# Performance work log

Measured on AMD Instinct MI355X. Metric: run time of the kernel, lower is better.

The kernel has to match this reference:

```python
import jax, jax.numpy as jnp
import numpy as np

D_MODEL = 512
N_HEAD = 8
D_K = 64
EPS = 1e-5


def setup_inputs() -> dict:
    key = jax.random.key(0)
    ks = jax.random.split(key, 12)
    B, S = 4, 2048
    Q = jax.random.normal(ks[0], (B, S, D_MODEL), dtype=jnp.float32)
    K = jax.random.normal(ks[1], (B, S, D_MODEL), dtype=jnp.float32)
    V = jax.random.normal(ks[2], (B, S, D_MODEL), dtype=jnp.float32)
    # bool padding-style mask: True = masked position
    att_mask = jax.random.randint(ks[3], (B, S, S), 0, 2).astype(bool)
    s = 1.0 / np.sqrt(D_MODEL)
    # Linear weights stored as [in, out] (transpose of torch's [out, in]; same math)
    Wq = jax.random.uniform(ks[4], (D_MODEL, N_HEAD * D_K), jnp.float32, -s, s)
    bq = jax.random.uniform(ks[5], (N_HEAD * D_K,), jnp.float32, -s, s)
    Wk = jax.random.uniform(ks[6], (D_MODEL, N_HEAD * D_K), jnp.float32, -s, s)
    bk = jax.random.uniform(ks[7], (N_HEAD * D_K,), jnp.float32, -s, s)
    Wv = jax.random.uniform(ks[8], (D_MODEL, N_HEAD * D_K), jnp.float32, -s, s)
    bv = jax.random.uniform(ks[9], (N_HEAD * D_K,), jnp.float32, -s, s)
    Wo = jax.random.uniform(ks[10], (N_HEAD * D_K, D_MODEL), jnp.float32, -s, s)
    bo = jax.random.uniform(ks[11], (D_MODEL,), jnp.float32, -s, s)
    return {"Q": Q, "K": K, "V": V, "att_mask": att_mask,
            "Wq": Wq, "bq": bq, "Wk": Wk, "bk": bk,
            "Wv": Wv, "bv": bv, "Wo": Wo, "bo": bo}


def _layer_norm(x):
    # nn.LayerNorm with default weight=1, bias=0 (fresh module in forward)
    mu = jnp.mean(x, axis=-1, keepdims=True)
    var = jnp.mean(jnp.square(x - mu), axis=-1, keepdims=True)
    return (x - mu) / jnp.sqrt(var + EPS)


def reference(Q, K, V, att_mask, Wq, bq, Wk, bk, Wv, bv, Wo, bo):
    B, S, _ = Q.shape
    residual = Q
    # QKV projections -> [B, H, S, Dk]
    q = (Q @ Wq + bq).reshape(B, S, N_HEAD, D_K).transpose(0, 2, 1, 3)
    k = (K @ Wk + bk).reshape(B, S, N_HEAD, D_K).transpose(0, 2, 1, 3)
    v = (V @ Wv + bv).reshape(B, S, N_HEAD, D_K).transpose(0, 2, 1, 3)
    # scaled dot-product attention with padding mask
    score = jnp.einsum('bhqd,bhkd->bhqk', q, k) / np.sqrt(D_K)
    score = jnp.where(att_mask[:, None, :, :], jnp.float32(-1e9), score)
    attn = jax.nn.softmax(score, axis=-1)
    context = jnp.einsum('bhqk,bhkd->bhqd', attn, v)
    context = context.transpose(0, 2, 1, 3).reshape(B, S, N_HEAD * D_K)
    output = context @ Wo + bo
    out = _layer_norm(output + residual)
    return out, attn
```

## Files before the change

kernel.cpp:

```cpp
#include <hip/hip_runtime.h>
#include <hip/hip_bf16.h>
#include <cstdint>
#include <cstddef>


typedef __attribute__((ext_vector_type(8)))  short short8v;
typedef __attribute__((ext_vector_type(2)))  float f32x2;
typedef __attribute__((ext_vector_type(4)))  float f32x4;
typedef __attribute__((ext_vector_type(16))) float f32x16;

constexpr int DM = 512, S = 2048, BATCH = 4, NHEAD = 8, DK = 64;
constexpr int ROWS = BATCH * S;
constexpr int BH   = BATCH * NHEAD;
constexpr size_t OUT_ELEMS = (size_t)ROWS * DM;
constexpr size_t HFRAG = 131072;

#define ZERO16 {0.f,0.f,0.f,0.f,0.f,0.f,0.f,0.f,0.f,0.f,0.f,0.f,0.f,0.f,0.f,0.f}

__device__ __forceinline__ unsigned short f2bf(float f) {
    union { __hip_bfloat16 b; unsigned short u; } c;
    c.b = __float2bfloat16(f);
    return c.u;
}
__device__ __forceinline__ float bf2f(unsigned short u) {
    union { float f; unsigned u32; } c;
    c.u32 = (unsigned)u << 16;
    return c.f;
}

__global__ __launch_bounds__(256)
void wconv(const float* __restrict__ Wq, const float* __restrict__ Wk,
           const float* __restrict__ Wv, const float* __restrict__ Wo,
           unsigned short* __restrict__ wt)
{
    __shared__ float T[32][33];
    const float* srcs[4] = {Wq, Wk, Wv, Wo};
    const float* W = srcs[blockIdx.z];
    unsigned short* out = wt + (size_t)blockIdx.z * DM * DM;
    const int r0 = blockIdx.y * 32, c0 = blockIdx.x * 32;
    const int tid = threadIdx.x;
#pragma unroll
    for (int i = 0; i < 4; ++i) {
        int lin = tid + i * 256; int r = lin >> 5, c = lin & 31;
        T[r][c] = W[(size_t)(r0 + r) * DM + c0 + c];
    }
    __syncthreads();
#pragma unroll
    for (int i = 0; i < 4; ++i) {
        int lin = tid + i * 256; int rn = lin >> 5, ck = lin & 31;
        out[(size_t)(c0 + rn) * DM + r0 + ck] = f2bf(T[ck][rn]);
    }
}

__global__ __launch_bounds__(256)
void maskpack(const uint8_t* __restrict__ mask, unsigned* __restrict__ mb)
{
    const int t = threadIdx.x;
    const int row = blockIdx.x * 4 + (t >> 6);
    const int w = t & 63;
    const uint8_t* src = mask + (size_t)row * S + 32 * w;
    const uint4 a = *reinterpret_cast<const uint4*>(src);
    const uint4 b = *reinterpret_cast<const uint4*>(src + 16);
    const unsigned m8[8] = {a.x, a.y, a.z, a.w, b.x, b.y, b.z, b.w};
    unsigned bits = 0;
#pragma unroll
    for (int k2 = 0; k2 < 32; ++k2)
        bits |= (((m8[k2 >> 2] >> (8 * (k2 & 3))) & 0xffu) ? 1u : 0u) << k2;
    mb[(size_t)row * 64 + w] = bits;
}

__global__ __launch_bounds__(256)
void proj3_mfma(const float* __restrict__ Qin, const float* __restrict__ Kin,
                const float* __restrict__ Vin, const unsigned short* __restrict__ wt,
                const float* __restrict__ bq, const float* __restrict__ bk,
                const float* __restrict__ bv,
                unsigned short* __restrict__ qo, unsigned short* __restrict__ ko,
                unsigned short* __restrict__ vo)
{
    const int z = blockIdx.z;
    const float* X = (z == 0) ? Qin : (z == 1) ? Kin : Vin;
    const unsigned short* Wt = wt + (size_t)z * DM * DM;
    const float* bias = (z == 0) ? bq : (z == 1) ? bk : bv;
    unsigned short* Y = (z == 0) ? qo : (z == 1) ? ko : vo;
    const float scale = (z == 0) ? 0.125f : 1.0f;

    const int tid = threadIdx.x, wv = tid >> 6, l = tid & 63, lr = l & 31, lh = l >> 5;
    const int m0 = blockIdx.y * 128 + wv * 32;
    const int n0 = blockIdx.x * 64;
    const float* xp = X + (size_t)(m0 + lr) * DM + 8 * lh;
    const unsigned short* w0 = Wt + (size_t)(n0 + lr) * DM + 8 * lh;
    const unsigned short* w1 = w0 + (size_t)32 * DM;
    f32x16 acc0 = ZERO16, acc1 = ZERO16;
#pragma unroll 8
    for (int t = 0; t < 32; ++t) {
        float4 xa = *reinterpret_cast<const float4*>(xp + 16 * t);
        float4 xb = *reinterpret_cast<const float4*>(xp + 16 * t + 4);
        short8v a;
        a[0] = (short)f2bf(xa.x * scale); a[1] = (short)f2bf(xa.y * scale);
        a[2] = (short)f2bf(xa.z * scale); a[3] = (short)f2bf(xa.w * scale);
        a[4] = (short)f2bf(xb.x * scale); a[5] = (short)f2bf(xb.y * scale);
        a[6] = (short)f2bf(xb.z * scale); a[7] = (short)f2bf(xb.w * scale);
        short8v b0 = *reinterpret_cast<const short8v*>(w0 + 16 * t);
        short8v b1 = *reinterpret_cast<const short8v*>(w1 + 16 * t);
        acc0 = __builtin_amdgcn_mfma_f32_32x32x16_bf16(a, b0, acc0, 0, 0, 0);
        acc1 = __builtin_amdgcn_mfma_f32_32x32x16_bf16(a, b1, acc1, 0, 0, 0);
    }
#pragma unroll
    for (int j = 0; j < 2; ++j) {
        const f32x16 acc = j ? acc1 : acc0;
        const int n = n0 + 32 * j + lr;
        const float bvv = bias[n] * scale;
        const int h = n >> 6, d = n & 63;
#pragma unroll
        for (int r = 0; r < 16; ++r) {
            const int m = m0 + (r & 3) + 8 * (r >> 2) + 4 * lh;
            const int bb = m >> 11, s = m & (S - 1);
            const int bh = bb * NHEAD + h;
            const unsigned short val = f2bf(acc[r] + bvv);
            size_t idx;
            if (z == 0)
                idx = ((size_t)bh * S + s) * DK + d;
            else if (z == 1)
                idx = (size_t)bh * HFRAG + (size_t)(s >> 4) * 1024 + (size_t)(d >> 5) * 512
                      + (size_t)(((s & 15) + 16 * ((d & 31) >> 3)) << 3) + (d & 7);
            else
                idx = (size_t)bh * HFRAG + (size_t)(s >> 5) * 2048 + (size_t)(d >> 4) * 512
                      + (size_t)(((d & 15) + 16 * ((s & 31) >> 3)) << 3) + (s & 7);
            Y[idx] = val;
        }
    }
}

__global__ __launch_bounds__(512)
void attn_fused(const unsigned short* __restrict__ q,
                const unsigned short* __restrict__ kpack,
                const unsigned short* __restrict__ vpack,
                const unsigned* __restrict__ mbits,
                float* __restrict__ attn,
                unsigned short* __restrict__ ctx)
{
    __shared__ char Pc[16 * 4096];
    __shared__ float cred[2][4][16][16];
    const int tid = threadIdx.x, wv = tid >> 6, l = tid & 63;
    const int lq = l & 15, lg = l >> 4;
    const int bh = blockIdx.y, q0 = blockIdx.x * 16;
    const int b = bh >> 3, h = bh & 7;

    const unsigned short* qp = q + ((size_t)bh * S + q0 + lq) * DK + 8 * lg;
    const short8v af0 = *reinterpret_cast<const short8v*>(qp);
    const short8v af1 = *reinterpret_cast<const short8v*>(qp + 32);
    const unsigned short* kbase = kpack + (size_t)bh * HFRAG + (size_t)l * 8;
#pragma unroll 4
    for (int it = 0; it < 16; ++it) {
        const int c = it * 8 + wv;
        const unsigned short* kc = kbase + (size_t)c * 1024;
        const short8v b0 = *reinterpret_cast<const short8v*>(kc);
        const short8v b1 = *reinterpret_cast<const short8v*>(kc + 512);
        f32x4 acc = {0.f, 0.f, 0.f, 0.f};
        acc = __builtin_amdgcn_mfma_f32_16x16x32_bf16(af0, b0, acc, 0, 0, 0);
        acc = __builtin_amdgcn_mfma_f32_16x16x32_bf16(af1, b1, acc, 0, 0, 0);
        const int col = c * 16 + lq;
#pragma unroll
        for (int r = 0; r < 4; ++r) {
            const int row = lg * 4 + r;
            *reinterpret_cast<unsigned short*>(
                Pc + row * 4096 + ((2 * col) ^ ((row & 7) << 4))) = f2bf(acc[r]);
        }
    }
    __syncthreads();

#pragma unroll
    for (int rr = 0; rr < 2; ++rr) {
        const int row = wv * 2 + rr;
        const int grow = q0 + row;
        const int swz = (row & 7) << 4;
        const unsigned mk = mbits[((size_t)b * S + grow) * 64 + l];
        float xs[4][8];
        float vmax = -1e30f;
#pragma unroll
        for (int i = 0; i < 4; ++i) {
            const int c = 4 * l + i;
            const short8v pr = *reinterpret_cast<const short8v*>(
                Pc + row * 4096 + ((16 * c) ^ swz));
#pragma unroll
            for (int j = 0; j < 8; ++j) {
                const bool masked = (mk >> (8 * i + j)) & 1u;
                xs[i][j] = masked ? -1e30f : bf2f((unsigned short)pr[j]);
                vmax = fmaxf(vmax, xs[i][j]);
            }
        }
#pragma unroll
        for (int off = 32; off; off >>= 1) vmax = fmaxf(vmax, __shfl_xor(vmax, off));
        float sum = 0.f;
#pragma unroll
        for (int i = 0; i < 4; ++i)
#pragma unroll
            for (int j = 0; j < 8; ++j) {
                xs[i][j] = __expf(xs[i][j] - vmax);
                sum += xs[i][j];
            }
#pragma unroll
        for (int off = 32; off; off >>= 1) sum += __shfl_xor(sum, off);
        const float inv = 1.0f / sum;
#pragma unroll
        for (int i = 0; i < 4; ++i) {
            const int c = 4 * l + i;
            ushort4 p0, p1;
            p0.x = f2bf(xs[i][0] * inv); p0.y = f2bf(xs[i][1] * inv);
            p0.z = f2bf(xs[i][2] * inv); p0.w = f2bf(xs[i][3] * inv);
            p1.x = f2bf(xs[i][4] * inv); p1.y = f2bf(xs[i][5] * inv);
            p1.z = f2bf(xs[i][6] * inv); p1.w = f2bf(xs[i][7] * inv);
            char* pb = Pc + row * 4096 + ((16 * c) ^ swz);
            *reinterpret_cast<ushort4*>(pb)     = p0;
            *reinterpret_cast<ushort4*>(pb + 8) = p1;
        }
    }
    __syncthreads();

    const int dt = wv & 3, kh = wv >> 2;
    const int rswz = (lq & 7) << 4;
    f32x4 acc = {0.f, 0.f, 0.f, 0.f};
    const unsigned short* vbase = vpack + (size_t)bh * HFRAG + dt * 512 + (size_t)l * 8;
    const int wrow = 8 * kh + 2 * dt + (l >> 5);
    const int wswz = (wrow & 7) << 4;
    const int lc = l & 31;
    float* arow = attn + ((size_t)bh * S + q0 + wrow) * S;
#pragma unroll 4
    for (int s = 0; s < 32; ++s) {
        const int kk0 = kh * 1024 + 32 * s;
        const short8v a = *reinterpret_cast<const short8v*>(
            Pc + lq * 4096 + ((2 * (kk0 + 8 * lg)) ^ rswz));
        const short8v bf = *reinterpret_cast<const short8v*>(
            vbase + (size_t)(kh * 32 + s) * 2048);
        acc = __builtin_amdgcn_mfma_f32_16x16x32_bf16(a, bf, acc, 0, 0, 0);
        const unsigned pw = *reinterpret_cast<const unsigned*>(
            Pc + wrow * 4096 + ((128 * s + 4 * lc) ^ wswz));
        f32x2 st;
        st[0] = bf2f((unsigned short)(pw & 0xffffu));
        st[1] = bf2f((unsigned short)(pw >> 16));
        __builtin_nontemporal_store(st,
            reinterpret_cast<f32x2*>(arow + 64 * s + 2 * lc));
    }
#pragma unroll
    for (int r = 0; r < 4; ++r) cred[kh][dt][lg * 4 + r][lq] = acc[r];
    __syncthreads();

    for (int o = tid; o < 1024; o += 512) {
        const int qq = o >> 6, dd = o & 63;
        const float val = cred[0][dd >> 4][qq][dd & 15] + cred[1][dd >> 4][qq][dd & 15];
        ctx[((size_t)(b * S + q0 + qq)) * DM + h * DK + dd] = f2bf(val);
    }
}

__global__ __launch_bounds__(256)
void out_mfma(const unsigned short* __restrict__ Xc, const unsigned short* __restrict__ Wt,
              const float* __restrict__ bias, const float* __restrict__ resid,
              float* __restrict__ pre)
{
    const int tid = threadIdx.x, wv = tid >> 6, l = tid & 63, lr = l & 31, lh = l >> 5;
    const int m0 = blockIdx.y * 128 + wv * 32;
    const int n0 = blockIdx.x * 64;
    const unsigned short* xp = Xc + (size_t)(m0 + lr) * DM + 8 * lh;
    const unsigned short* w0 = Wt + (size_t)(n0 + lr) * DM + 8 * lh;
    const unsigned short* w1 = w0 + (size_t)32 * DM;
    f32x16 acc0 = ZERO16, acc1 = ZERO16;
#pragma unroll 8
    for (int t = 0; t < 32; ++t) {
        short8v a  = *reinterpret_cast<const short8v*>(xp + 16 * t);
        short8v b0 = *reinterpret_cast<const short8v*>(w0 + 16 * t);
        short8v b1 = *reinterpret_cast<const short8v*>(w1 + 16 * t);
        acc0 = __builtin_amdgcn_mfma_f32_32x32x16_bf16(a, b0, acc0, 0, 0, 0);
        acc1 = __builtin_amdgcn_mfma_f32_32x32x16_bf16(a, b1, acc1, 0, 0, 0);
    }
#pragma unroll
    for (int j = 0; j < 2; ++j) {
        const f32x16 acc = j ? acc1 : acc0;
        const int n = n0 + 32 * j + lr;
        const float bv = bias[n];
#pragma unroll
        for (int r = 0; r < 16; ++r) {
            const int m = m0 + (r & 3) + 8 * (r >> 2) + 4 * lh;
            pre[(size_t)m * DM + n] = acc[r] + bv + resid[(size_t)m * DM + n];
        }
    }
}

__global__ __launch_bounds__(128)
void ln_kernel(const float* __restrict__ pre, float* __restrict__ out)
{
    const size_t row = blockIdx.x;
    const int tid = threadIdx.x;
    const int wave = tid >> 6;
    float4 x = reinterpret_cast<const float4*>(pre + row * DM)[tid];

    float s = x.x + x.y + x.z + x.w;
#pragma unroll
    for (int off = 32; off; off >>= 1) s += __shfl_xor(s, off);
    __shared__ float r1[2];
    if ((tid & 63) == 0) r1[wave] = s;
    __syncthreads();
    const float mean = (r1[0] + r1[1]) * (1.0f / 512.0f);

    float dx = x.x - mean, dy = x.y - mean, dz = x.z - mean, dw = x.w - mean;
    float sq = dx * dx + dy * dy + dz * dz + dw * dw;
#pragma unroll
    for (int off = 32; off; off >>= 1) sq += __shfl_xor(sq, off);
    __shared__ float r2[2];
    if ((tid & 63) == 0) r2[wave] = sq;
    __syncthreads();
    const float var = (r2[0] + r2[1]) * (1.0f / 512.0f);
    const float inv = rsqrtf(var + 1e-5f);

    float4 y;
    y.x = dx * inv; y.y = dy * inv; y.z = dz * inv; y.w = dw * inv;
    reinterpret_cast<float4*>(out + row * DM)[tid] = y;
}

extern "C" void kernel_launch(void* const* d_in, const int* in_sizes, int n_in,
                              void* d_out, int out_size, void* d_ws, size_t ws_size,
                              hipStream_t stream)
{
    (void)in_sizes; (void)n_in; (void)out_size; (void)ws_size;

    const float*   Qin  = (const float*)d_in[0];
    const float*   Kin  = (const float*)d_in[1];
    const float*   Vin  = (const float*)d_in[2];
    const uint8_t* mask = (const uint8_t*)d_in[3];
    const float*   Wq   = (const float*)d_in[4];
    const float*   bq   = (const float*)d_in[5];
    const float*   Wk   = (const float*)d_in[6];
    const float*   bk   = (const float*)d_in[7];
    const float*   Wv   = (const float*)d_in[8];
    const float*   bv   = (const float*)d_in[9];
    const float*   Wo   = (const float*)d_in[10];
    const float*   bo   = (const float*)d_in[11];

    float* out  = (float*)d_out;
    float* attn = out + OUT_ELEMS;

    char* w = (char*)d_ws;
    const size_t MB = 1 << 20;
    unsigned short* wt    = (unsigned short*)(w);
    unsigned short* qbf   = (unsigned short*)(w + 2  * MB);
    unsigned short* kpack = (unsigned short*)(w + 10 * MB);
    unsigned short* vpack = (unsigned short*)(w + 18 * MB);
    unsigned short* ctx   = (unsigned short*)(w + 26 * MB);
    float*          pre   = (float*)(w + 34 * MB);
    unsigned*       mbits = (unsigned*)(w + 50 * MB);

    unsigned short* wto = wt + 3 * (size_t)DM * DM;

    wconv<<<dim3(16, 16, 4), 256, 0, stream>>>(Wq, Wk, Wv, Wo, wt);

    maskpack<<<ROWS / 4, 256, 0, stream>>>(mask, mbits);

    proj3_mfma<<<dim3(DM / 64, ROWS / 128, 3), 256, 0, stream>>>(
        Qin, Kin, Vin, wt, bq, bk, bv, qbf, kpack, vpack);

    attn_fused<<<dim3(S / 16, BH), 512, 0, stream>>>(qbf, kpack, vpack, mbits, attn, ctx);

    out_mfma<<<dim3(DM / 64, ROWS / 128), 256, 0, stream>>>(ctx, wto, bo, Qin, pre);

    ln_kernel<<<ROWS, 128, 0, stream>>>(pre, out);
}
```

Baseline: 325.5 us.

## Keep attention scores in registers and fuse output projection with LayerNorm

The attention kernel now computes QK^T with K as the A operand, so each wave holds a 16x256 slice of scores in registers. Masking and softmax run in registers, with a cross-wave max/sum reduction through small shared arrays. The fp32 attention probabilities are written directly from registers, which drops the bf16 round-trip through LDS and the extra pass that reloaded scores for the store. Separately, the output projection and LayerNorm are fused into one kernel that covers a full 512-wide row per block, removing the fp32 pre-activation buffer. Variance now comes from a single pass as E[x^2]-mean^2, which carries some cancellation risk, and the 64 accumulator registers per lane may add register pressure despite the launch-bounds hint.

```diff
diff --git a/kernel.cpp b/kernel.cpp
--- a/kernel.cpp
+++ b/kernel.cpp
@@ -131,7 +131,7 @@
     }
 }
 
-__global__ __launch_bounds__(512)
+__global__ __launch_bounds__(512, 4)
 void attn_fused(const unsigned short* __restrict__ q,
                 const unsigned short* __restrict__ kpack,
                 const unsigned short* __restrict__ vpack,
@@ -141,90 +141,90 @@
 {
     __shared__ char Pc[16 * 4096];
     __shared__ float cred[2][4][16][16];
+    __shared__ float redm[8][16];
+    __shared__ float reds[8][16];
     const int tid = threadIdx.x, wv = tid >> 6, l = tid & 63;
     const int lq = l & 15, lg = l >> 4;
     const int bh = blockIdx.y, q0 = blockIdx.x * 16;
     const int b = bh >> 3, h = bh & 7;
 
     const unsigned short* qp = q + ((size_t)bh * S + q0 + lq) * DK + 8 * lg;
-    const short8v af0 = *reinterpret_cast<const short8v*>(qp);
-    const short8v af1 = *reinterpret_cast<const short8v*>(qp + 32);
+    const short8v qf0 = *reinterpret_cast<const short8v*>(qp);
+    const short8v qf1 = *reinterpret_cast<const short8v*>(qp + 32);
     const unsigned short* kbase = kpack + (size_t)bh * HFRAG + (size_t)l * 8;
-#pragma unroll 4
+    f32x4 acc[16];
+#pragma unroll
     for (int it = 0; it < 16; ++it) {
-        const int c = it * 8 + wv;
-        const unsigned short* kc = kbase + (size_t)c * 1024;
-        const short8v b0 = *reinterpret_cast<const short8v*>(kc);
-        const short8v b1 = *reinterpret_cast<const short8v*>(kc + 512);
-        f32x4 acc = {0.f, 0.f, 0.f, 0.f};
-        acc = __builtin_amdgcn_mfma_f32_16x16x32_bf16(af0, b0, acc, 0, 0, 0);
-        acc = __builtin_amdgcn_mfma_f32_16x16x32_bf16(af1, b1, acc, 0, 0, 0);
-        const int col = c * 16 + lq;
+        const unsigned short* kc = kbase + (size_t)(16 * wv + it) * 1024;
+        const short8v kf0 = *reinterpret_cast<const short8v*>(kc);
+        const short8v kf1 = *reinterpret_cast<const short8v*>(kc + 512);
+        f32x4 a = {0.f, 0.f, 0.f, 0.f};
+        a = __builtin_amdgcn_mfma_f32_16x16x32_bf16(kf0, qf0, a, 0, 0, 0);
+        a = __builtin_amdgcn_mfma_f32_16x16x32_bf16(kf1, qf1, a, 0, 0, 0);
+        acc[it] = a;
+    }
+
+    const unsigned* mrow = mbits + ((size_t)b * S + q0 + lq) * 64 + 8 * wv;
+    const uint4 mwa = *reinterpret_cast<const uint4*>(mrow);
+    const uint4 mwb = *reinterpret_cast<const uint4*>(mrow + 4);
+    const unsigned mw[8] = {mwa.x, mwa.y, mwa.z, mwa.w, mwb.x, mwb.y, mwb.z, mwb.w};
+    float vmax = -3e38f;
+#pragma unroll
+    for (int it = 0; it < 16; ++it) {
+        const unsigned word = mw[it >> 1] >> (16 * (it & 1) + 4 * lg);
 #pragma unroll
         for (int r = 0; r < 4; ++r) {
-            const int row = lg * 4 + r;
-            *reinterpret_cast<unsigned short*>(
-                Pc + row * 4096 + ((2 * col) ^ ((row & 7) << 4))) = f2bf(acc[r]);
+            const float v = ((word >> r) & 1u) ? -1e30f : acc[it][r];
+            acc[it][r] = v;
+            vmax = fmaxf(vmax, v);
         }
     }
-    __syncthreads();
-
-#pragma unroll
-    for (int rr = 0; rr < 2; ++rr) {
-        const int row = wv * 2 + rr;
-        const int grow = q0 + row;
-        const int swz = (row & 7) << 4;
-        const unsigned mk = mbits[((size_t)b * S + grow) * 64 + l];
-        float xs[4][8];
-        float vmax = -1e30f;
-#pragma unroll
-        for (int i = 0; i < 4; ++i) {
-            const int c = 4 * l + i;
-            const short8v pr = *reinterpret_cast<const short8v*>(
-                Pc + row * 4096 + ((16 * c) ^ swz));
-#pragma unroll
-            for (int j = 0; j < 8; ++j) {
-                const bool masked = (mk >> (8 * i + j)) & 1u;
-                xs[i][j] = masked ? -1e30f : bf2f((unsigned short)pr[j]);
-                vmax = fmaxf(vmax, xs[i][j]);
-            }
+    vmax = fmaxf(vmax, __shfl_xor(vmax, 16));
+    vmax = fmaxf(vmax, __shfl_xor(vmax, 32));
+    if (l < 16) redm[wv][l] = vmax;
+    __syncthreads();
+    float rmax = redm[0][lq];
+#pragma unroll
+    for (int w2 = 1; w2 < 8; ++w2) rmax = fmaxf(rmax, redm[w2][lq]);
+
+    float sum = 0.f;
+#pragma unroll
+    for (int it = 0; it < 16; ++it)
+#pragma unroll
+        for (int r = 0; r < 4; ++r) {
+            const float v = __expf(acc[it][r] - rmax);
+            acc[it][r] = v;
+            sum += v;
         }
-#pragma unroll
-        for (int off = 32; off; off >>= 1) vmax = fmaxf(vmax, __shfl_xor(vmax, off));
-        float sum = 0.f;
-#pragma unroll
-        for (int i = 0; i < 4; ++i)
-#pragma unroll
-            for (int j = 0; j < 8; ++j) {
-                xs[i][j] = __expf(xs[i][j] - vmax);
-                sum += xs[i][j];
-            }
-#pragma unroll
-        for (int off = 32; off; off >>= 1) sum += __shfl_xor(sum, off);
-        const float inv = 1.0f / sum;
-#pragma unroll
-        for (int i = 0; i < 4; ++i) {
-            const int c = 4 * l + i;
-            ushort4 p0, p1;
-            p0.x = f2bf(xs[i][0] * inv); p0.y = f2bf(xs[i][1] * inv);
-            p0.z = f2bf(xs[i][2] * inv); p0.w = f2bf(xs[i][3] * inv);
-            p1.x = f2bf(xs[i][4] * inv); p1.y = f2bf(xs[i][5] * inv);
-            p1.z = f2bf(xs[i][6] * inv); p1.w = f2bf(xs[i][7] * inv);
-            char* pb = Pc + row * 4096 + ((16 * c) ^ swz);
-            *reinterpret_cast<ushort4*>(pb)     = p0;
-            *reinterpret_cast<ushort4*>(pb + 8) = p1;
-        }
+    sum += __shfl_xor(sum, 16);
+    sum += __shfl_xor(sum, 32);
+    if (l < 16) reds[wv][l] = sum;
+    __syncthreads();
+    float rsum = 0.f;
+#pragma unroll
+    for (int w2 = 0; w2 < 8; ++w2) rsum += reds[w2][lq];
+    const float inv = 1.0f / rsum;
+
+    float* arow = attn + ((size_t)bh * S + q0 + lq) * S + 256 * wv;
+    const int swz = (lq & 7) << 4;
+    char* prow = Pc + lq * 4096;
+#pragma unroll
+    for (int it = 0; it < 16; ++it) {
+        const int n = 16 * it + 4 * lg;
+        f32x4 o;
+        o[0] = acc[it][0] * inv; o[1] = acc[it][1] * inv;
+        o[2] = acc[it][2] * inv; o[3] = acc[it][3] * inv;
+        __builtin_nontemporal_store(o, reinterpret_cast<f32x4*>(arow + n));
+        ushort4 p;
+        p.x = f2bf(o[0]); p.y = f2bf(o[1]); p.z = f2bf(o[2]); p.w = f2bf(o[3]);
+        *reinterpret_cast<ushort4*>(prow + ((2 * (256 * wv + n)) ^ swz)) = p;
     }
     __syncthreads();
 
     const int dt = wv & 3, kh = wv >> 2;
     const int rswz = (lq & 7) << 4;
-    f32x4 acc = {0.f, 0.f, 0.f, 0.f};
+    f32x4 pacc = {0.f, 0.f, 0.f, 0.f};
     const unsigned short* vbase = vpack + (size_t)bh * HFRAG + dt * 512 + (size_t)l * 8;
-    const int wrow = 8 * kh + 2 * dt + (l >> 5);
-    const int wswz = (wrow & 7) << 4;
-    const int lc = l & 31;
-    float* arow = attn + ((size_t)bh * S + q0 + wrow) * S;
 #pragma unroll 4
     for (int s = 0; s < 32; ++s) {
         const int kk0 = kh * 1024 + 32 * s;
@@ -232,17 +232,10 @@
             Pc + lq * 4096 + ((2 * (kk0 + 8 * lg)) ^ rswz));
         const short8v bf = *reinterpret_cast<const short8v*>(
             vbase + (size_t)(kh * 32 + s) * 2048);
-        acc = __builtin_amdgcn_mfma_f32_16x16x32_bf16(a, bf, acc, 0, 0, 0);
-        const unsigned pw = *reinterpret_cast<const unsigned*>(
-            Pc + wrow * 4096 + ((128 * s + 4 * lc) ^ wswz));
-        f32x2 st;
-        st[0] = bf2f((unsigned short)(pw & 0xffffu));
-        st[1] = bf2f((unsigned short)(pw >> 16));
-        __builtin_nontemporal_store(st,
-            reinterpret_cast<f32x2*>(arow + 64 * s + 2 * lc));
-    }
-#pragma unroll
-    for (int r = 0; r < 4; ++r) cred[kh][dt][lg * 4 + r][lq] = acc[r];
+        pacc = __builtin_amdgcn_mfma_f32_16x16x32_bf16(a, bf, pacc, 0, 0, 0);
+    }
+#pragma unroll
+    for (int r = 0; r < 4; ++r) cred[kh][dt][lg * 4 + r][lq] = pacc[r];
     __syncthreads();
 
     for (int o = tid; o < 1024; o += 512) {
@@ -252,14 +245,16 @@
     }
 }
 
-__global__ __launch_bounds__(256)
-void out_mfma(const unsigned short* __restrict__ Xc, const unsigned short* __restrict__ Wt,
-              const float* __restrict__ bias, const float* __restrict__ resid,
-              float* __restrict__ pre)
-{
+__global__ __launch_bounds__(512)
+void out_ln(const unsigned short* __restrict__ Xc, const unsigned short* __restrict__ Wt,
+            const float* __restrict__ bias, const float* __restrict__ resid,
+            float* __restrict__ out)
+{
+    __shared__ f32x2 red[32][8];
+    __shared__ f32x2 stat[32];
     const int tid = threadIdx.x, wv = tid >> 6, l = tid & 63, lr = l & 31, lh = l >> 5;
-    const int m0 = blockIdx.y * 128 + wv * 32;
-    const int n0 = blockIdx.x * 64;
+    const int m0 = blockIdx.x * 32;
+    const int n0 = wv * 64;
     const unsigned short* xp = Xc + (size_t)(m0 + lr) * DM + 8 * lh;
     const unsigned short* w0 = Wt + (size_t)(n0 + lr) * DM + 8 * lh;
     const unsigned short* w1 = w0 + (size_t)32 * DM;
@@ -272,48 +267,41 @@
         acc0 = __builtin_amdgcn_mfma_f32_32x32x16_bf16(a, b0, acc0, 0, 0, 0);
         acc1 = __builtin_amdgcn_mfma_f32_32x32x16_bf16(a, b1, acc1, 0, 0, 0);
     }
-#pragma unroll
-    for (int j = 0; j < 2; ++j) {
-        const f32x16 acc = j ? acc1 : acc0;
-        const int n = n0 + 32 * j + lr;
-        const float bv = bias[n];
-#pragma unroll
-        for (int r = 0; r < 16; ++r) {
-            const int m = m0 + (r & 3) + 8 * (r >> 2) + 4 * lh;
-            pre[(size_t)m * DM + n] = acc[r] + bv + resid[(size_t)m * DM + n];
+    const float bv0 = bias[n0 + lr], bv1 = bias[n0 + 32 + lr];
+#pragma unroll
+    for (int r = 0; r < 16; ++r) {
+        const int mloc = (r & 3) + 8 * (r >> 2) + 4 * lh;
+        const size_t mbase = (size_t)(m0 + mloc) * DM + n0 + lr;
+        const float v0 = acc0[r] + bv0 + resid[mbase];
+        const float v1 = acc1[r] + bv1 + resid[mbase + 32];
+        acc0[r] = v0; acc1[r] = v1;
+        float s = v0 + v1, sq = v0 * v0 + v1 * v1;
+#pragma unroll
+        for (int off = 16; off; off >>= 1) {
+            s  += __shfl_xor(s, off);
+            sq += __shfl_xor(sq, off);
         }
-    }
-}
-
-__global__ __launch_bounds__(128)
-void ln_kernel(const float* __restrict__ pre, float* __restrict__ out)
-{
-    const size_t row = blockIdx.x;
-    const int tid = threadIdx.x;
-    const int wave = tid >> 6;
-    float4 x = reinterpret_cast<const float4*>(pre + row * DM)[tid];
-
-    float s = x.x + x.y + x.z + x.w;
-#pragma unroll
-    for (int off = 32; off; off >>= 1) s += __shfl_xor(s, off);
-    __shared__ float r1[2];
-    if ((tid & 63) == 0) r1[wave] = s;
-    __syncthreads();
-    const float mean = (r1[0] + r1[1]) * (1.0f / 512.0f);
-
-    float dx = x.x - mean, dy = x.y - mean, dz = x.z - mean, dw = x.w - mean;
-    float sq = dx * dx + dy * dy + dz * dz + dw * dw;
-#pragma unroll
-    for (int off = 32; off; off >>= 1) sq += __shfl_xor(sq, off);
-    __shared__ float r2[2];
-    if ((tid & 63) == 0) r2[wave] = sq;
-    __syncthreads();
-    const float var = (r2[0] + r2[1]) * (1.0f / 512.0f);
-    const float inv = rsqrtf(var + 1e-5f);
-
-    float4 y;
-    y.x = dx * inv; y.y = dy * inv; y.z = dz * inv; y.w = dw * inv;
-    reinterpret_cast<float4*>(out + row * DM)[tid] = y;
+        if (lr == 0) { f32x2 t2; t2[0] = s; t2[1] = sq; red[mloc][wv] = t2; }
+    }
+    __syncthreads();
+    if (tid < 32) {
+        float s = 0.f, sq = 0.f;
+#pragma unroll
+        for (int w2 = 0; w2 < 8; ++w2) { s += red[tid][w2][0]; sq += red[tid][w2][1]; }
+        const float mean = s * (1.0f / 512.0f);
+        const float var = sq * (1.0f / 512.0f) - mean * mean;
+        f32x2 t2; t2[0] = mean; t2[1] = rsqrtf(var + 1e-5f);
+        stat[tid] = t2;
+    }
+    __syncthreads();
+#pragma unroll
+    for (int r = 0; r < 16; ++r) {
+        const int mloc = (r & 3) + 8 * (r >> 2) + 4 * lh;
+        const f32x2 st = stat[mloc];
+        const size_t mbase = (size_t)(m0 + mloc) * DM + n0 + lr;
+        out[mbase]      = (acc0[r] - st[0]) * st[1];
+        out[mbase + 32] = (acc1[r] - st[0]) * st[1];
+    }
 }
 
 extern "C" void kernel_launch(void* const* d_in, const int* in_sizes, int n_in,
@@ -345,8 +333,7 @@
     unsigned short* kpack = (unsigned short*)(w + 10 * MB);
     unsigned short* vpack = (unsigned short*)(w + 18 * MB);
     unsigned short* ctx   = (unsigned short*)(w + 26 * MB);
-    float*          pre   = (float*)(w + 34 * MB);
-    unsigned*       mbits = (unsigned*)(w + 50 * MB);
+    unsigned*       mbits = (unsigned*)(w + 34 * MB);
 
     unsigned short* wto = wt + 3 * (size_t)DM * DM;
 
@@ -359,7 +346,5 @@
 
     attn_fused<<<dim3(S / 16, BH), 512, 0, stream>>>(qbf, kpack, vpack, mbits, attn, ctx);
 
-    out_mfma<<<dim3(DM / 64, ROWS / 128), 256, 0, stream>>>(ctx, wto, bo, Qin, pre);
-
-    ln_kernel<<<ROWS, 128, 0, stream>>>(pre, out);
-}
+    out_ln<<<ROWS / 32, 512, 0, stream>>>(ctx, wto, bo, Qin, out);
+}
```

After: 365.1 us. +12.2%, slower.
